# Performance work log

Measured on AMD Instinct MI355X. Metric: run time of the kernel, lower is better.

The kernel has to match this reference:

```python
import jax, jax.numpy as jnp
import numpy as np

P = 1  # padding (= kernel_size // 2 for 3x3 convs), matches init_kwargs


def _rot(a, k):
    # torch x.rot90(k, dims=(-2, -1)) equivalent
    return jnp.rot90(a, k, axes=(-2, -1))


def _tl(p, top, lft):
    # interpolated top-left corner for equatorial faces (no shared pixel)
    ret = jnp.zeros(top.shape[:-2] + (p, p), top.dtype)
    ret = ret.at[..., -1, -1].set(0.5 * top[..., -1, 0] + 0.5 * lft[..., 0, -1])
    for i in range(1, p):
        ret = ret.at[..., -i - 1, -i:].set(top[..., -i - 1, :i])
        ret = ret.at[..., -i:, -i - 1].set(lft[..., :i, -i - 1])
        ret = ret.at[..., -i - 1, -i - 1].set(0.5 * top[..., -i - 1, 0] + 0.5 * lft[..., 0, -i - 1])
    return ret


def _br(p, b, r):
    # interpolated bottom-right corner for equatorial faces
    ret = jnp.zeros(b.shape[:-2] + (p, p), b.dtype)
    ret = ret.at[..., 0, 0].set(0.5 * b[..., 0, -1] + 0.5 * r[..., -1, 0])
    for i in range(1, p):
        ret = ret.at[..., :i, i].set(r[..., -i:, i])
        ret = ret.at[..., i, :i].set(b[..., i, -i:])
        ret = ret.at[..., i, i].set(0.5 * b[..., i, -1] + 0.5 * r[..., -1, i])
    return ret


def _pn(p, c, t, tl, lft, bl, b, br, rgt, tr):
    # north polar face: top neighbour rotated +90deg, top-left +180deg
    c = jnp.concatenate([_rot(t, 1)[..., -p:, :], c, b[..., :p, :]], axis=-2)
    left = jnp.concatenate([_rot(tl, 2)[..., -p:, -p:], _rot(lft, -1)[..., -p:], bl[..., :p, -p:]], axis=-2)
    right = jnp.concatenate([tr[..., -p:, :p], rgt[..., :p], br[..., :p, :p]], axis=-2)
    return jnp.concatenate([left, c, right], axis=-1)


def _pe(p, c, t, tl, lft, bl, b, br, rgt, tr):
    # equatorial face: no rotations
    c = jnp.concatenate([t[..., -p:, :], c, b[..., :p, :]], axis=-2)
    left = jnp.concatenate([tl[..., -p:, -p:], lft[..., -p:], bl[..., :p, -p:]], axis=-2)
    right = jnp.concatenate([tr[..., -p:, :p], rgt[..., :p], br[..., :p, :p]], axis=-2)
    return jnp.concatenate([left, c, right], axis=-1)


def _ps(p, c, t, tl, lft, bl, b, br, rgt, tr):
    # south polar face: bottom +90deg, right -90deg, bottom-right +180deg
    c = jnp.concatenate([t[..., -p:, :], c, _rot(b, 1)[..., :p, :]], axis=-2)
    left = jnp.concatenate([tl[..., -p:, -p:], lft[..., -p:], bl[..., :p, -p:]], axis=-2)
    right = jnp.concatenate([tr[..., -p:, :p], _rot(rgt, -1)[..., :p], _rot(br, 2)[..., :p, :p]], axis=-2)
    return jnp.concatenate([left, c, right], axis=-1)


def _healpix_pad(x, p):
    B12, C, n, _ = x.shape
    x5 = x.reshape(B12 // 12, 12, C, n, n)  # (B, 12, C, n, n)
    f = [x5[:, i] for i in range(12)]
    pads = [
        _pn(p, f[0], f[1], f[2], f[3], f[3], f[4], f[8], f[5], f[1]),
        _pn(p, f[1], f[2], f[3], f[0], f[0], f[5], f[9], f[6], f[2]),
        _pn(p, f[2], f[3], f[0], f[1], f[1], f[6], f[10], f[7], f[3]),
        _pn(p, f[3], f[0], f[1], f[2], f[2], f[7], f[11], f[4], f[0]),
        _pe(p, f[4], f[0], _tl(p, f[0], f[3]), f[3], f[7], f[11], _br(p, f[11], f[8]), f[8], f[5]),
        _pe(p, f[5], f[1], _tl(p, f[1], f[0]), f[0], f[4], f[8], _br(p, f[8], f[9]), f[9], f[6]),
        _pe(p, f[6], f[2], _tl(p, f[2], f[1]), f[1], f[5], f[9], _br(p, f[9], f[10]), f[10], f[7]),
        _pe(p, f[7], f[3], _tl(p, f[3], f[2]), f[2], f[6], f[10], _br(p, f[10], f[11]), f[11], f[4]),
        _ps(p, f[8], f[5], f[0], f[4], f[11], f[11], f[10], f[9], f[9]),
        _ps(p, f[9], f[6], f[1], f[5], f[8], f[8], f[11], f[10], f[10]),
        _ps(p, f[10], f[7], f[2], f[6], f[9], f[9], f[8], f[11], f[11]),
        _ps(p, f[11], f[4], f[3], f[7], f[10], f[10], f[9], f[8], f[8]),
    ]
    out = jnp.stack(pads, axis=1)  # (B, 12, C, n+2p, n+2p)
    return out.reshape(B12, C, n + 2 * p, n + 2 * p)


def setup_inputs() -> dict:
    key = jax.random.key(0)
    x = jax.random.normal(key, (24, 128, 128, 128), dtype=jnp.float32)
    return {"x": x}


def reference(x):
    return _healpix_pad(x, P)
```

## Files before the change

### kernel.cpp

```cpp
#include <hip/hip_runtime.h>


#define NPLANE_OUT 16900

__device__ __forceinline__ float hp_face(const float* __restrict__ in, size_t baseoff,
                                         int q, int i, int j) {
  return in[baseoff + ((size_t)q << 21) + (i << 7) + j];
}

__device__ __forceinline__ float hp_val(const float* __restrict__ in, size_t baseoff,
                                        int type, int m, int face, int r, int col) {
  const int L = 127;
  if (r == 0) {
    if (col == 0) {
      if (type == 0) return hp_face(in, baseoff, (m + 2) & 3, 0, 0);
      if (type == 1) return 0.5f * (hp_face(in, baseoff, m, L, 0) +
                                    hp_face(in, baseoff, (m + 3) & 3, 0, L));
      return hp_face(in, baseoff, m, L, L);
    }
    if (col == 129) {
      if (type == 0) return hp_face(in, baseoff, (m + 1) & 3, L, 0);
      if (type == 1) return hp_face(in, baseoff, 4 + ((m + 1) & 3), L, 0);
      return hp_face(in, baseoff, 8 + ((m + 1) & 3), L, 0);
    }
    int j = col - 1;
    if (type == 0) return hp_face(in, baseoff, (m + 1) & 3, j, 0);
    if (type == 1) return hp_face(in, baseoff, m, L, j);
    return hp_face(in, baseoff, 4 + ((m + 1) & 3), L, j);
  }
  if (r == 129) {
    if (col == 0) {
      if (type == 0) return hp_face(in, baseoff, (m + 3) & 3, 0, L);
      if (type == 1) return hp_face(in, baseoff, 4 + ((m + 3) & 3), 0, L);
      return hp_face(in, baseoff, 8 + ((m + 3) & 3), 0, L);
    }
    if (col == 129) {
      if (type == 0) return hp_face(in, baseoff, 8 + m, 0, 0);
      if (type == 1) return 0.5f * (hp_face(in, baseoff, 8 + ((m + 3) & 3), 0, L) +
                                    hp_face(in, baseoff, 8 + m, L, 0));
      return hp_face(in, baseoff, 8 + ((m + 2) & 3), L, L);
    }
    int j = col - 1;
    if (type == 0) return hp_face(in, baseoff, 4 + m, 0, j);
    if (type == 1) return hp_face(in, baseoff, 8 + ((m + 3) & 3), 0, j);
    return hp_face(in, baseoff, 8 + ((m + 3) & 3), j, L);
  }
  int i = r - 1;
  if (col == 0) {
    if (type == 0) return hp_face(in, baseoff, (m + 3) & 3, 0, i);
    if (type == 1) return hp_face(in, baseoff, (m + 3) & 3, i, L);
    return hp_face(in, baseoff, 4 + m, i, L);
  }
  if (type == 0) return hp_face(in, baseoff, 4 + ((m + 1) & 3), i, 0);
  if (type == 1) return hp_face(in, baseoff, 8 + m, i, 0);
  return hp_face(in, baseoff, 8 + ((m + 1) & 3), L, i);
}

typedef float f4v __attribute__((ext_vector_type(4)));

__global__ __launch_bounds__(256) void CREDITHEALPix_90975997264316_kernel(
    const float* __restrict__ in, float* __restrict__ out) {
  int plane = blockIdx.x;
  int b12 = plane >> 7;
  int c = plane & 127;
  int batch = (b12 >= 12) ? 1 : 0;
  int face = b12 - batch * 12;
  int type = face >> 2;
  int m = face & 3;
  size_t baseoff = (((size_t)batch * 1536) + (size_t)c) << 14;
  const float* __restrict__ src = in + baseoff + ((size_t)face << 21);
  float* __restrict__ oplane = out + (size_t)plane * NPLANE_OUT;

  for (int t4 = threadIdx.x; t4 < 4225; t4 += 256) {
    int e = t4 << 2;
    int r = e / 130;
    int col = e - r * 130;
    f4v v;
    if (r >= 1 && r <= 128 && col >= 1 && col <= 125) {
      const float* __restrict__ p = src + ((r - 1) << 7) + (col - 1);
      v[0] = p[0];
      v[1] = p[1];
      v[2] = p[2];
      v[3] = p[3];
    } else {
      #pragma unroll
      for (int k = 0; k < 4; ++k) {
        int ek = e + k;
        int rk = ek / 130;
        int ck = ek - rk * 130;
        if (rk == 0 || rk == 129 || ck == 0 || ck == 129) {
          v[k] = hp_val(in, baseoff, type, m, face, rk, ck);
        } else {
          v[k] = src[((rk - 1) << 7) + (ck - 1)];
        }
      }
    }
    *(f4v*)(oplane + e) = v;
  }
}

extern "C" void kernel_launch(void* const* d_in, const int* in_sizes, int n_in,
                              void* d_out, int out_size, void* d_ws, size_t ws_size,
                              hipStream_t stream) {
  const float* in = (const float*)d_in[0];
  float* out = (float*)d_out;
  dim3 grid(3072, 1, 1);
  dim3 block(256, 1, 1);
  CREDITHEALPix_90975997264316_kernel<<<grid, block, 0, stream>>>(in, out);
}
```

Measured before the change: 379.6 us.

## Replace per-element halo branching with precomputed gather index table

```diff
diff --git a/kernel.cpp b/kernel.cpp
--- a/kernel.cpp
+++ b/kernel.cpp
@@ -2,14 +2,141 @@
 
 
 #define NPLANE_OUT 16900
+#define TAB_ELEMS  (12 * NPLANE_OUT)
+
+__device__ __forceinline__ int hp_fidx(int q, int i, int j) {
+  return (q << 21) + (i << 7) + j;
+}
+
+__device__ int hp_idx(int type, int m, int face, int r, int col) {
+  const int L = 127;
+  if (r == 0) {
+    if (col == 0) {
+      if (type == 0) return hp_fidx((m + 2) & 3, 0, 0);
+      if (type == 1) return hp_fidx(m, L, 0);
+      return hp_fidx(m, L, L);
+    }
+    if (col == 129) {
+      if (type == 0) return hp_fidx((m + 1) & 3, L, 0);
+      if (type == 1) return hp_fidx(4 + ((m + 1) & 3), L, 0);
+      return hp_fidx(8 + ((m + 1) & 3), L, 0);
+    }
+    int j = col - 1;
+    if (type == 0) return hp_fidx((m + 1) & 3, j, 0);
+    if (type == 1) return hp_fidx(m, L, j);
+    return hp_fidx(4 + ((m + 1) & 3), L, j);
+  }
+  if (r == 129) {
+    if (col == 0) {
+      if (type == 0) return hp_fidx((m + 3) & 3, 0, L);
+      if (type == 1) return hp_fidx(4 + ((m + 3) & 3), 0, L);
+      return hp_fidx(8 + ((m + 3) & 3), 0, L);
+    }
+    if (col == 129) {
+      if (type == 0) return hp_fidx(8 + m, 0, 0);
+      if (type == 1) return hp_fidx(8 + ((m + 3) & 3), 0, L);
+      return hp_fidx(8 + ((m + 2) & 3), L, L);
+    }
+    int j = col - 1;
+    if (type == 0) return hp_fidx(4 + m, 0, j);
+    if (type == 1) return hp_fidx(8 + ((m + 3) & 3), 0, j);
+    return hp_fidx(8 + ((m + 3) & 3), j, L);
+  }
+  int i = r - 1;
+  if (col == 0) {
+    if (type == 0) return hp_fidx((m + 3) & 3, 0, i);
+    if (type == 1) return hp_fidx((m + 3) & 3, i, L);
+    return hp_fidx(4 + m, i, L);
+  }
+  if (col == 129) {
+    if (type == 0) return hp_fidx(4 + ((m + 1) & 3), i, 0);
+    if (type == 1) return hp_fidx(8 + m, i, 0);
+    return hp_fidx(8 + ((m + 1) & 3), L, i);
+  }
+  return (face << 21) + ((r - 1) << 7) + (col - 1);
+}
+
+__global__ __launch_bounds__(256) void hp_build_table(int* __restrict__ tab) {
+  int idx = blockIdx.x * 256 + threadIdx.x;
+  if (idx >= TAB_ELEMS) return;
+  int face = idx / NPLANE_OUT;
+  int e = idx - face * NPLANE_OUT;
+  int r = e / 130;
+  int col = e - r * 130;
+  tab[idx] = hp_idx(face >> 2, face & 3, face, r, col);
+}
+
+typedef float f4v __attribute__((ext_vector_type(4)));
+typedef int   i4v __attribute__((ext_vector_type(4)));
+
+__global__ __launch_bounds__(256) void CREDITHEALPix_90975997264316_kernel(
+    const float* __restrict__ in, const int* __restrict__ tab,
+    float* __restrict__ out) {
+  int q0 = blockIdx.x * 1024 + threadIdx.x;
+
+  i4v tq[4];
+  size_t inbase[4];
+  #pragma unroll
+  for (int k = 0; k < 4; ++k) {
+    int Q = q0 + (k << 8);
+    int plane = Q / 4225;
+    int t4 = Q - plane * 4225;
+    int b12 = plane >> 7;
+    int c = plane & 127;
+    int batch = (b12 >= 12) ? 1 : 0;
+    int face = b12 - batch * 12;
+    inbase[k] = (((size_t)(batch ? 1536 : 0)) + (size_t)c) << 14;
+    tq[k] = *(const i4v*)(tab + face * NPLANE_OUT + (t4 << 2));
+  }
+  f4v v[4];
+  #pragma unroll
+  for (int k = 0; k < 4; ++k) {
+    const float* __restrict__ b = in + inbase[k];
+    v[k][0] = b[tq[k][0]];
+    v[k][1] = b[tq[k][1]];
+    v[k][2] = b[tq[k][2]];
+    v[k][3] = b[tq[k][3]];
+  }
+  #pragma unroll
+  for (int k = 0; k < 4; ++k) {
+    *(f4v*)(out + ((size_t)(q0 + (k << 8)) << 2)) = v[k];
+  }
+}
+
+__global__ __launch_bounds__(256) void hp_patch_corners(
+    const float* __restrict__ in, float* __restrict__ out) {
+  int t = blockIdx.x * 256 + threadIdx.x;
+  if (t >= 2048) return;
+  int corner = t & 1;
+  int pl = t >> 1;
+  int batch = (pl >= 512) ? 1 : 0;
+  int rem = pl - batch * 512;
+  int m = rem >> 7;
+  int c = rem & 127;
+  int b12 = batch * 12 + 4 + m;
+  int plane = (b12 << 7) + c;
+  size_t baseoff = (((size_t)batch * 1536) + (size_t)c) << 14;
+  float v;
+  int e;
+  if (corner == 0) {
+    v = 0.5f * (in[baseoff + hp_fidx(m, 127, 0)] +
+                in[baseoff + hp_fidx((m + 3) & 3, 0, 127)]);
+    e = 0;
+  } else {
+    v = 0.5f * (in[baseoff + hp_fidx(8 + ((m + 3) & 3), 0, 127)] +
+                in[baseoff + hp_fidx(8 + m, 127, 0)]);
+    e = NPLANE_OUT - 1;
+  }
+  out[(size_t)plane * NPLANE_OUT + e] = v;
+}
 
 __device__ __forceinline__ float hp_face(const float* __restrict__ in, size_t baseoff,
                                          int q, int i, int j) {
   return in[baseoff + ((size_t)q << 21) + (i << 7) + j];
 }
 
-__device__ __forceinline__ float hp_val(const float* __restrict__ in, size_t baseoff,
-                                        int type, int m, int face, int r, int col) {
+__device__ float hp_val(const float* __restrict__ in, size_t baseoff,
+                        int type, int m, int face, int r, int col) {
   const int L = 127;
   if (r == 0) {
     if (col == 0) {
@@ -56,9 +183,7 @@
   return hp_face(in, baseoff, 8 + ((m + 1) & 3), L, i);
 }
 
-typedef float f4v __attribute__((ext_vector_type(4)));
-
-__global__ __launch_bounds__(256) void CREDITHEALPix_90975997264316_kernel(
+__global__ __launch_bounds__(256) void hp_fallback_kernel(
     const float* __restrict__ in, float* __restrict__ out) {
   int plane = blockIdx.x;
   int b12 = plane >> 7;
@@ -78,10 +203,7 @@
     f4v v;
     if (r >= 1 && r <= 128 && col >= 1 && col <= 125) {
       const float* __restrict__ p = src + ((r - 1) << 7) + (col - 1);
-      v[0] = p[0];
-      v[1] = p[1];
-      v[2] = p[2];
-      v[3] = p[3];
+      v[0] = p[0]; v[1] = p[1]; v[2] = p[2]; v[3] = p[3];
     } else {
       #pragma unroll
       for (int k = 0; k < 4; ++k) {
@@ -104,7 +226,12 @@
                               hipStream_t stream) {
   const float* in = (const float*)d_in[0];
   float* out = (float*)d_out;
-  dim3 grid(3072, 1, 1);
-  dim3 block(256, 1, 1);
-  CREDITHEALPix_90975997264316_kernel<<<grid, block, 0, stream>>>(in, out);
-}
+  if (ws_size >= (size_t)TAB_ELEMS * sizeof(int)) {
+    int* tab = (int*)d_ws;
+    hp_build_table<<<dim3((TAB_ELEMS + 255) / 256), dim3(256), 0, stream>>>(tab);
+    CREDITHEALPix_90975997264316_kernel<<<dim3(12675), dim3(256), 0, stream>>>(in, tab, out);
+    hp_patch_corners<<<dim3(8), dim3(256), 0, stream>>>(in, out);
+  } else {
+    hp_fallback_kernel<<<dim3(3072), dim3(256), 0, stream>>>(in, out);
+  }
+}
```

After: 344.6 us. 9.2% less time.
